# Optimization experiments

Measured on AMD Instinct MI355X. Metric: run time of the kernel, lower is better.

Reference implementation:

```python
import jax, jax.numpy as jnp
import numpy as np
import math

B, Hs, Ws, C, NH, PP = 4, 32, 32, 1024, 16, 128
N = Hs * Ws
HD = C // NH
MAX_REL = 32
ROPE_THETA = 10000.0


def _gelu(t):
    return jax.nn.gelu(t, approximate=False)  # torch nn.GELU default (erf)


def _rope(x):
    # x: [B, nh, N, hd]; interleaved even/odd rotation as in _apply_rope
    hd = x.shape[-1]
    inv_freq = 1.0 / (ROPE_THETA ** (jnp.arange(0, hd, 2, dtype=jnp.float32) / hd))
    pos = jnp.arange(x.shape[-2], dtype=jnp.float32)
    ang = pos[:, None] * inv_freq[None, :]  # [N, hd/2]
    sin, cos = jnp.sin(ang), jnp.cos(ang)
    x1, x2 = x[..., 0::2], x[..., 1::2]
    return jnp.stack([x1 * cos - x2 * sin, x2 * cos + x1 * sin], axis=-1).reshape(x.shape)


def _rel_bias(table):
    # static index computation (numpy), gather from learned table -> [1, NH, N, N]
    coords = np.arange(Hs)
    cy, cx = np.meshgrid(coords, coords, indexing='ij')
    cf = np.stack([cy.reshape(-1), cx.reshape(-1)])  # [2, N]
    rel = cf[:, :, None] - cf[:, None, :]            # [2, N, N]
    idx = (rel[0] + MAX_REL - 1) * (2 * MAX_REL - 1) + (rel[1] + MAX_REL - 1)
    return table[jnp.asarray(idx.reshape(-1))].reshape(N, N, NH).transpose(2, 0, 1)[None]


def setup_inputs() -> dict:
    key = jax.random.key(0)
    ks = iter(jax.random.split(key, 40))
    def w(shape, s=0.02):
        return jax.random.normal(next(ks), shape, jnp.float32) * s
    return dict(
        x=jax.random.normal(next(ks), (B, N, C), jnp.float32),
        plucker=jax.random.normal(next(ks), (B, Hs, Ws, 6), jnp.float32),
        w_qkv=w((C, 3 * C)), w_self_proj=w((C, C)), b_self_proj=jnp.zeros((C,), jnp.float32),
        pl_w1=w((6, 2 * PP)), pl_b1=jnp.zeros((2 * PP,), jnp.float32),
        pl_w2=w((2 * PP, PP)), pl_b2=jnp.zeros((PP,), jnp.float32),
        pl_w3=w((PP, PP)), pl_b3=jnp.zeros((PP,), jnp.float32),
        w_cq=w((C, C)), w_pk=w((PP, C)), w_pv=w((PP, C)),
        w_cross_proj=w((C, C)), b_cross_proj=jnp.zeros((C,), jnp.float32),
        ray_dir_bias=w((NH,)),
        ds_w1=w((6, 4 * NH)), ds_b1=jnp.zeros((4 * NH,), jnp.float32),
        ds_w2=w((4 * NH, NH)), ds_b2=jnp.zeros((NH,), jnp.float32),
        gb_w1=w((2 * PP, C // 2)), gb_b1=jnp.zeros((C // 2,), jnp.float32),
        gb_w2=w((C // 2, NH)), gb_b2=jnp.zeros((NH,), jnp.float32),
        rel_table=w(((2 * MAX_REL - 1) ** 2, NH)),
        gfe_w1=w((C + PP, C)), gfe_b1=jnp.zeros((C,), jnp.float32),
        gfe_w2=w((C, C)), gfe_b2=jnp.zeros((C,), jnp.float32),
    )


def reference(x, plucker, w_qkv, w_self_proj, b_self_proj,
              pl_w1, pl_b1, pl_w2, pl_b2, pl_w3, pl_b3,
              w_cq, w_pk, w_pv, w_cross_proj, b_cross_proj,
              ray_dir_bias, ds_w1, ds_b1, ds_w2, ds_b2,
              gb_w1, gb_b1, gb_w2, gb_b2, rel_table,
              gfe_w1, gfe_b1, gfe_w2, gfe_b2):
    scale = HD ** (-0.5)
    pl_flat = plucker.reshape(B, N, 6)

    # ---- self attention with RoPE + relative position bias ----
    qkv = (x @ w_qkv).reshape(B, N, 3, NH, HD).transpose(2, 0, 3, 1, 4)
    q, k, v = qkv[0], qkv[1], qkv[2]          # [B, NH, N, HD]
    q, k = _rope(q), _rope(k)
    attn = jnp.einsum('bhnd,bhmd->bhnm', q, k) * scale + _rel_bias(rel_table)
    attn = jax.nn.softmax(attn, axis=-1)
    sa = jnp.einsum('bhnm,bhmd->bhnd', attn, v).transpose(0, 2, 1, 3).reshape(B, N, C)
    sa = sa @ w_self_proj + b_self_proj

    # ---- plucker mlp embedding ----
    pp = _gelu(pl_flat @ pl_w1 + pl_b1)
    pp = _gelu(pp @ pl_w2 + pl_b2)
    pp = pp @ pl_w3 + pl_b3                   # [B, N, PP]

    # ---- cross attention (features -> plucker) with geometric biases ----
    cq = (sa @ w_cq).reshape(B, N, NH, HD).transpose(0, 2, 1, 3)
    ck = (pp @ w_pk).reshape(B, N, NH, HD).transpose(0, 2, 1, 3)
    cv = (pp @ w_pv).reshape(B, N, NH, HD).transpose(0, 2, 1, 3)
    cq, ck = _rope(cq), _rope(ck)
    ca = jnp.einsum('bhnd,bhmd->bhnm', cq, ck) * scale

    # ray direction similarity bias (per-head learned weight)
    d = pl_flat[..., :3]
    dn = d / jnp.maximum(jnp.linalg.norm(d, axis=-1, keepdims=True), 1e-12)
    sim = jnp.einsum('bnd,bmd->bnm', dn, dn)  # [B, N, N]
    ca = ca + sim[:, None, :, :] * ray_dir_bias[None, :, None, None]

    # distance-aware per-query multiplicative scale
    ds = jnp.tanh(_gelu(pl_flat @ ds_w1 + ds_b1) @ ds_w2 + ds_b2)  # [B, N, NH]
    ca = ca * (1.0 + ds.transpose(0, 2, 1)[..., None])

    # geometric attention bias from spatial diffs of plucker features
    p2 = pp.reshape(B, Hs, Ws, PP)
    hdiff = jnp.pad(jnp.abs(p2[:, :, 1:] - p2[:, :, :-1]), ((0, 0), (0, 0), (0, 1), (0, 0)))
    vdiff = jnp.pad(jnp.abs(p2[:, 1:] - p2[:, :-1]), ((0, 0), (0, 1), (0, 0), (0, 0)))
    sd = jnp.concatenate([hdiff, vdiff], axis=-1).reshape(B, N, 2 * PP)
    gb = jnp.tanh(_gelu(sd @ gb_w1 + gb_b1) @ gb_w2 + gb_b2)  # [B, N, NH]
    ca = ca + gb.transpose(0, 2, 1)[:, :, None, :]            # broadcast over queries

    ca = jax.nn.softmax(ca, axis=-1)
    co = jnp.einsum('bhnm,bhmd->bhnd', ca, cv).transpose(0, 2, 1, 3).reshape(B, N, C)
    co = co @ w_cross_proj + b_cross_proj

    # ---- geometric feature enhancement + residual ----
    enh = _gelu(jnp.concatenate([co, pp], axis=-1) @ gfe_w1 + gfe_b1) @ gfe_w2 + gfe_b2
    return enh + x
```

## Files before the change

kernel.cpp:

```cpp
#include <hip/hip_runtime.h>
#include <math.h>

#define B_ 4
#define N_ 1024
#define C_ 1024
#define NH_ 16
#define HD_ 64
#define PP_ 128
#define LOG2E 1.4426950408889634f

typedef __bf16 bf16;
typedef __attribute__((ext_vector_type(8))) __bf16 bf16x8;
typedef __attribute__((ext_vector_type(4))) __bf16 bf16x4;
typedef __attribute__((ext_vector_type(4))) float f32x4;

#define MFMA_BF16(a, b, c) __builtin_amdgcn_mfma_f32_16x16x32_bf16((a), (b), (c), 0, 0, 0)

__device__ __forceinline__ float gelu_f(float x) {
    return 0.5f * x * (1.0f + erff(x * 0.70710678118654752f));
}

__device__ __forceinline__ void gload16(const void* g, void* l) {
    __builtin_amdgcn_global_load_lds(
        (const __attribute__((address_space(1))) void*)g,
        (__attribute__((address_space(3))) void*)l, 16, 0, 0);
}

__device__ __forceinline__ void stage64(const bf16* __restrict__ g, int pitchB,
                                        bf16* lds, int t) {
    int row = t >> 3, c = t & 7;
    const char* src = (const char*)g + (size_t)row * pitchB + ((c ^ (row & 7)) << 4);
    gload16(src, lds + (size_t)(t & 448) * 8);
}

__device__ __forceinline__ void stage32(const bf16* __restrict__ g, bf16* lds, int t) {
    if (t < 256) {
        int row = t >> 3, c = t & 7;
        const char* src = (const char*)g + (size_t)row * 128 + ((c ^ (row & 7)) << 4);
        gload16(src, lds + (size_t)(t & 192) * 8);
    }
}

__device__ __forceinline__ bf16x8 lds8_swz(const bf16* lds, int row, int colb) {
    return *reinterpret_cast<const bf16x8*>(
        (const char*)lds + row * 128 + (colb ^ ((row & 7) << 4)));
}

__device__ __forceinline__ bf16x8 lds8_swz256(const bf16* lds, int row, int colb) {
    return *reinterpret_cast<const bf16x8*>(
        (const char*)lds + row * 256 + (colb ^ ((row & 7) << 4)));
}

__device__ __forceinline__ bf16x8 lds8_ke(const bf16* lds, int kr, int g) {
    int r = kr >> 1;
    int ch = ((kr & 1) * 4 + g) ^ (r & 7);
    return *reinterpret_cast<const bf16x8*>((const char*)lds + r * 128 + (ch << 4));
}

__global__ __launch_bounds__(256) void rope_tab_k(float2* __restrict__ rt)
{
    int g = blockIdx.x * 256 + threadIdx.x;
    const int n = g >> 5, i = g & 31;
    const float inv = powf(10000.0f, -(float)(2 * i) / 64.0f);
    const float ang = (float)n * inv;
    rt[g] = make_float2(cosf(ang), sinf(ang));
}

__global__ __launch_bounds__(256) void relT_k(const float* __restrict__ rel_table,
                                              float* __restrict__ relT)
{
    int g = blockIdx.x * 256 + threadIdx.x;
    if (g >= 16 * 3969) return;
    int h = g / 3969, idx = g - h * 3969;
    relT[g] = rel_table[idx * 16 + h];
}

struct TJobs {
    const float* src[11];
    bf16* dst[11];
    int K[11];
    int N[11];
};

__global__ __launch_bounds__(256) void tcast_k(TJobs J)
{
    const int j = blockIdx.z;
    const int Kd = J.K[j], Nd = J.N[j];
    const int n0 = blockIdx.x * 32, k0 = blockIdx.y * 32;
    if (n0 >= Nd || k0 >= Kd) return;
    __shared__ float tl[32][33];
    const int t = threadIdx.x, tx = t & 31, ty = t >> 5;
    const float* src = J.src[j];
    bf16* dst = J.dst[j];
    #pragma unroll
    for (int r = 0; r < 4; ++r) {
        int kk = ty + r * 8;
        tl[kk][tx] = src[(size_t)(k0 + kk) * Nd + n0 + tx];
    }
    __syncthreads();
    #pragma unroll
    for (int r = 0; r < 4; ++r) {
        int nn = ty + r * 8;
        dst[(size_t)(n0 + nn) * Kd + k0 + tx] = (bf16)tl[tx][nn];
    }
}

__global__ __launch_bounds__(256) void cast_rm(const float* __restrict__ in,
                                               bf16* __restrict__ out, int n4)
{
    int g = blockIdx.x * 256 + threadIdx.x;
    if (g >= n4) return;
    float4 v = reinterpret_cast<const float4*>(in)[g];
    bf16x4 o = {(bf16)v.x, (bf16)v.y, (bf16)v.z, (bf16)v.w};
    reinterpret_cast<bf16x4*>(out)[g] = o;
}

template<int NI, int BK>
__global__ __launch_bounds__(256) void gemm_m(
    const bf16* __restrict__ A, const bf16* __restrict__ A2,
    const bf16* __restrict__ Bt, const bf16* __restrict__ Bt2,
    const float* __restrict__ bias, const float* __restrict__ resid,
    void* __restrict__ out0, void* __restrict__ out1, void* __restrict__ out2,
    const float2* __restrict__ rtab,
    int M, int N, int K, int K1A, int K1B, int epi, int act_gelu, float scale)
{
    __shared__ bf16 As[2][128 * BK];
    __shared__ bf16 Bs[2][NI * 32 * BK];
    const int t = threadIdx.x;
    const int w = t >> 6, lane = t & 63;
    const int row0 = blockIdx.y * 128, col0 = blockIdx.x * (NI * 32);
    const int wm = w >> 1, wn = w & 1;
    const int K2A = K - K1A, K2B = K - K1B;
    f32x4 acc[4][NI];
    #pragma unroll
    for (int mi = 0; mi < 4; ++mi)
        #pragma unroll
        for (int ni = 0; ni < NI; ++ni)
            acc[mi][ni] = (f32x4){0.f, 0.f, 0.f, 0.f};

    #define STAGE_AB32(k0, buf)                                                \
        {                                                                      \
            _Pragma("unroll")                                                  \
            for (int r = 0; r < 2; ++r) {                                      \
                int c = r * 256 + t;                                           \
                int rr = c >> 2, koff = (c & 3) * 8;                           \
                const bf16* srca = ((k0) < K1A)                                \
                    ? A + (size_t)(row0 + rr) * K1A + (k0) + koff              \
                    : A2 + (size_t)(row0 + rr) * K2A + ((k0) - K1A) + koff;    \
                gload16(srca, As[buf] + (size_t)(r * 256 + (t & 192)) * 8);    \
            }                                                                  \
            _Pragma("unroll")                                                  \
            for (int r = 0; r < NI / 2; ++r) {                                 \
                int c = r * 256 + t;                                           \
                int rr = c >> 2, koff = (c & 3) * 8;                           \
                const bf16* srcb = ((k0) < K1B)                                \
                    ? Bt + (size_t)(col0 + rr) * K1B + (k0) + koff             \
                    : Bt2 + (size_t)(col0 + rr) * K2B + ((k0) - K1B) + koff;   \
                gload16(srcb, Bs[buf] + (size_t)(r * 256 + (t & 192)) * 8);    \
            }                                                                  \
        }

    #define STAGE_AB64(k0, buf)                                                \
        {                                                                      \
            const bf16* abase; int apitch;                                     \
            if ((k0) < K1A) { abase = A + (k0); apitch = K1A; }                \
            else            { abase = A2 + ((k0) - K1A); apitch = K2A; }       \
            _Pragma("unroll")                                                  \
            for (int r = 0; r < 4; ++r) {                                      \
                int c = r * 256 + t;                                           \
                int rr = c >> 3, cc = c & 7;                                   \
                const char* srca = (const char*)(abase + (size_t)(row0 + rr) * apitch) \
                                   + ((cc ^ (rr & 7)) << 4);                   \
                gload16(srca, As[buf] + (size_t)(r * 256 + (t & 192)) * 8);    \
            }                                                                  \
            const bf16* bbase; int bpitch;                                     \
            if ((k0) < K1B) { bbase = Bt + (k0); bpitch = K1B; }               \
            else            { bbase = Bt2 + ((k0) - K1B); bpitch = K2B; }      \
            _Pragma("unroll")                                                  \
            for (int r = 0; r < NI; ++r) {                                     \
                int c = r * 256 + t;                                           \
                int rr = c >> 3, cc = c & 7;                                   \
                const char* srcb = (const char*)(bbase + (size_t)(col0 + rr) * bpitch) \
                                   + ((cc ^ (rr & 7)) << 4);                   \
                gload16(srcb, Bs[buf] + (size_t)(r * 256 + (t & 192)) * 8);    \
            }                                                                  \
        }

    int cur = 0;
    const int nk = K / BK;
    if constexpr (BK == 32) {
        STAGE_AB32(0, 0);
        __syncthreads();
        for (int kk = 0; kk < nk; ++kk) {
            if (kk + 1 < nk) STAGE_AB32((kk + 1) * 32, cur ^ 1);
            bf16x8 af[4], bfv[NI];
            #pragma unroll
            for (int mi = 0; mi < 4; ++mi)
                af[mi] = *reinterpret_cast<const bf16x8*>(
                    As[cur] + (wm * 64 + mi * 16 + (lane & 15)) * 32 + (lane >> 4) * 8);
            #pragma unroll
            for (int ni = 0; ni < NI; ++ni)
                bfv[ni] = *reinterpret_cast<const bf16x8*>(
                    Bs[cur] + (wn * (NI * 16) + ni * 16 + (lane & 15)) * 32 + (lane >> 4) * 8);
            #pragma unroll
            for (int mi = 0; mi < 4; ++mi)
                #pragma unroll
                for (int ni = 0; ni < NI; ++ni)
                    acc[mi][ni] = MFMA_BF16(af[mi], bfv[ni], acc[mi][ni]);
            __syncthreads();
            cur ^= 1;
        }
    } else {
        STAGE_AB64(0, 0);
        __syncthreads();
        for (int kk = 0; kk < nk; ++kk) {
            if (kk + 1 < nk) STAGE_AB64((kk + 1) * 64, cur ^ 1);
            bf16x8 af[4][2], bfv[NI][2];
            #pragma unroll
            for (int mi = 0; mi < 4; ++mi)
                #pragma unroll
                for (int kh = 0; kh < 2; ++kh)
                    af[mi][kh] = lds8_swz(As[cur], wm * 64 + mi * 16 + (lane & 15),
                                          kh * 64 + (lane >> 4) * 16);
            #pragma unroll
            for (int ni = 0; ni < NI; ++ni)
                #pragma unroll
                for (int kh = 0; kh < 2; ++kh)
                    bfv[ni][kh] = lds8_swz(Bs[cur], wn * (NI * 16) + ni * 16 + (lane & 15),
                                           kh * 64 + (lane >> 4) * 16);
            #pragma unroll
            for (int kh = 0; kh < 2; ++kh)
                #pragma unroll
                for (int mi = 0; mi < 4; ++mi)
                    #pragma unroll
                    for (int ni = 0; ni < NI; ++ni)
                        acc[mi][ni] = MFMA_BF16(af[mi][kh], bfv[ni][kh], acc[mi][ni]);
            __syncthreads();
            cur ^= 1;
        }
    }
    #undef STAGE_AB32
    #undef STAGE_AB64

    #pragma unroll
    for (int mi = 0; mi < 4; ++mi) {
        #pragma unroll
        for (int ni = 0; ni < NI; ++ni) {
            const int col = col0 + wn * (NI * 16) + ni * 16 + (lane & 15);
            if (epi <= 1 || epi == 5) {
                const float bv = bias ? bias[col] : 0.f;
                #pragma unroll
                for (int j = 0; j < 4; ++j) {
                    const int row = row0 + wm * 64 + mi * 16 + (lane >> 4) * 4 + j;
                    float v = acc[mi][ni][j] + bv;
                    if (act_gelu) v = gelu_f(v);
                    if (epi == 0) {
                        if (resid) v += resid[(size_t)row * N + col];
                        ((float*)out0)[(size_t)row * N + col] = v;
                    } else if (epi == 1) {
                        ((bf16*)out0)[(size_t)row * N + col] = (bf16)v;
                    } else {
                        ((float*)out0)[(size_t)row * N + col] = v;
                        ((bf16*)out1)[(size_t)row * N + col] = (bf16)v;
                    }
                }
            } else if (epi == 2) {
                const int reg = col >> 10;
                const int h = (col >> 6) & 15, d = col & 63;
                if (reg <= 1) {
                    bf16* dst = reg == 0 ? (bf16*)out0 : (bf16*)out1;
                    const float sc = reg == 0 ? scale : 1.0f;
                    #pragma unroll
                    for (int j = 0; j < 4; ++j) {
                        const int row = row0 + wm * 64 + mi * 16 + (lane >> 4) * 4 + j;
                        const int b = row >> 10, n = row & 1023;
                        float v = acc[mi][ni][j];
                        float pv = __shfl_xor(v, 1);
                        float2 cs = rtab[(n << 5) + (d >> 1)];
                        float o = (d & 1) == 0 ? v * cs.x - pv * cs.y
                                               : v * cs.x + pv * cs.y;
                        dst[((size_t)((b * 16 + h) * 1024 + n)) * 64 + d] = (bf16)(o * sc);
                    }
                } else {
                    bf16x4 o4;
                    #pragma unroll
                    for (int j = 0; j < 4; ++j) o4[j] = (bf16)acc[mi][ni][j];
                    const int row = row0 + wm * 64 + mi * 16 + (lane >> 4) * 4;
                    const int b = row >> 10, n = row & 1023;
                    *reinterpret_cast<bf16x4*>(
                        (bf16*)out2 + ((size_t)((b * 16 + h) * 64 + d)) * 1024 + n) = o4;
                }
            } else if (epi == 3 || epi == 6) {
                const int h = (col >> 6) & 15, d = col & 63;
                const float bv = bias ? bias[col] : 0.f;
                #pragma unroll
                for (int j = 0; j < 4; ++j) {
                    const int row = row0 + wm * 64 + mi * 16 + (lane >> 4) * 4 + j;
                    const int b = row >> 10, n = row & 1023;
                    float v = acc[mi][ni][j] + bv;
                    float pv = __shfl_xor(v, 1);
                    float2 cs = rtab[(n << 5) + (d >> 1)];
                    float o = (d & 1) == 0 ? v * cs.x - pv * cs.y
                                           : v * cs.x + pv * cs.y;
                    float sc = scale;
                    if (epi == 6) sc *= 1.0f + resid[(size_t)row * 16 + h];
                    ((bf16*)out0)[((size_t)((b * 16 + h) * 1024 + n)) * 64 + d] = (bf16)(o * sc);
                }
            } else if (epi == 7) {
                const int reg = col >> 10;
                const int h = (col >> 6) & 15, d = col & 63;
                if (reg == 0) {
                    #pragma unroll
                    for (int j = 0; j < 4; ++j) {
                        const int row = row0 + wm * 64 + mi * 16 + (lane >> 4) * 4 + j;
                        const int b = row >> 10, n = row & 1023;
                        float v = acc[mi][ni][j];
                        float pv = __shfl_xor(v, 1);
                        float2 cs = rtab[(n << 5) + (d >> 1)];
                        float o = (d & 1) == 0 ? v * cs.x - pv * cs.y
                                               : v * cs.x + pv * cs.y;
                        ((bf16*)out0)[((size_t)((b * 16 + h) * 1024 + n)) * 64 + d] = (bf16)o;
                    }
                } else {
                    bf16x4 o4;
                    #pragma unroll
                    for (int j = 0; j < 4; ++j) o4[j] = (bf16)acc[mi][ni][j];
                    const int row = row0 + wm * 64 + mi * 16 + (lane >> 4) * 4;
                    const int b = row >> 10, n = row & 1023;
                    *reinterpret_cast<bf16x4*>(
                        (bf16*)out2 + ((size_t)((b * 16 + h) * 64 + d)) * 1024 + n) = o4;
                }
            } else {
                const int h = (col >> 6) & 15, d = col & 63;
                bf16x4 o4;
                #pragma unroll
                for (int j = 0; j < 4; ++j) o4[j] = (bf16)acc[mi][ni][j];
                const int row = row0 + wm * 64 + mi * 16 + (lane >> 4) * 4;
                const int b = row >> 10, n = row & 1023;
                *reinterpret_cast<bf16x4*>(
                    (bf16*)out0 + ((size_t)((b * 16 + h) * 64 + d)) * 1024 + n) = o4;
            }
        }
    }
}

__device__ __forceinline__ void attn_bid(int bid, int& bh, int& r0t) {
    const int xcd = bid & 7, s = bid >> 3;
    bh = (s >> 3) * 8 + xcd;
    r0t = s & 7;
}

__global__ __launch_bounds__(512) void attn_self_m(
    const bf16* __restrict__ qb, const bf16* __restrict__ kb, const bf16* __restrict__ vtb,
    const float* __restrict__ relT, bf16* __restrict__ sab)
{
    __shared__ bf16 Ks[2][64 * 64];
    __shared__ bf16 Vs[2][80 * 64];
    __shared__ bf16 Ps[128 * 64];
    __shared__ float relb[2][320];
    const int t = threadIdx.x, w = t >> 6, lane = t & 63;
    int bh, r0t;
    attn_bid(blockIdx.x, bh, r0t);
    const int b = bh >> 4, h = bh & 15, r0 = r0t * 128;
    const float* relTh = relT + h * 3969;
    const int y0 = r0 >> 5;

    {
        const bf16* g = qb + ((size_t)bh * 1024 + r0) * 64;
        #pragma unroll
        for (int r = 0; r < 2; ++r) {
            int i = r * 512 + t;
            int row = i >> 3, c = i & 7;
            const char* src = (const char*)g + (size_t)row * 128 + ((c ^ (row & 7)) << 4);
            gload16(src, Ps + (size_t)(r * 512 + (t & 448)) * 8);
        }
    }
    __syncthreads();
    bf16x8 aq[2];
    {
        const int qr = w * 16 + (lane & 15);
        aq[0] = lds8_swz(Ps, qr, (lane >> 4) * 16);
        aq[1] = lds8_swz(Ps, qr, 64 + (lane >> 4) * 16);
    }
    for (int i = t; i < 2048; i += 512) {
        int buf = i >> 10, idx = i & 1023;
        int row = 64 + (idx >> 6), col = idx & 63;
        Vs[buf][row * 64 + col] = (row == 64) ? (bf16)1.0f : (bf16)0.0f;
    }
    __syncthreads();
    stage64(kb + (size_t)bh * 65536, 128, Ks[0], t);
    stage64(vtb + (size_t)bh * 65536, 2048, Vs[0], t);
    if (t < 320) relb[0][t] = LOG2E * relTh[(y0 + 30 + (t >> 6)) * 63 + min(t & 63, 62)];

    float m_run[4];
    f32x4 of[4], ofe;
    #pragma unroll
    for (int j = 0; j < 4; ++j) m_run[j] = -3e38f;
    #pragma unroll
    for (int dt = 0; dt < 4; ++dt) of[dt] = (f32x4){0.f, 0.f, 0.f, 0.f};
    ofe = (f32x4){0.f, 0.f, 0.f, 0.f};

    const int qrow_lo = (lane >> 4) * 4;
    int dybase[4];
    #pragma unroll
    for (int j = 0; j < 4; ++j) {
        int qg = r0 + w * 16 + qrow_lo + j;
        dybase[j] = (((qg >> 5) - y0) + 1) * 64 + (qg & 31) + 31;
    }
    __syncthreads();

    int cur = 0;
    for (int mt = 0; mt < 16; ++mt) {
        if (mt < 15) {
            stage64(kb + (size_t)bh * 65536 + (size_t)(mt + 1) * 64 * 64, 128, Ks[cur ^ 1], t);
            stage64(vtb + (size_t)bh * 65536 + (size_t)(mt + 1) * 64, 2048, Vs[cur ^ 1], t);
            if (t < 320)
                relb[cur ^ 1][t] = LOG2E * relTh[(y0 - 2 * (mt + 1) + 30 + (t >> 6)) * 63 + min(t & 63, 62)];
        }
        f32x4 sf[4];
        __builtin_amdgcn_s_setprio(1);
        #pragma unroll
        for (int ct = 0; ct < 4; ++ct) {
            const int kr = ct * 16 + (lane & 15);
            f32x4 a = (f32x4){0.f, 0.f, 0.f, 0.f};
            a = MFMA_BF16(aq[0], lds8_swz(Ks[cur], kr, (lane >> 4) * 16), a);
            a = MFMA_BF16(aq[1], lds8_swz(Ks[cur], kr, 64 + (lane >> 4) * 16), a);
            sf[ct] = a;
        }
        __builtin_amdgcn_s_setprio(0);
        float p[4][4], lmax[4];
        #pragma unroll
        for (int j = 0; j < 4; ++j) lmax[j] = -3e38f;
        #pragma unroll
        for (int ct = 0; ct < 4; ++ct) {
            const int xm = (ct & 1) * 16 + (lane & 15);
            const int ro = (ct >> 1) * 64 + xm;
            #pragma unroll
            for (int j = 0; j < 4; ++j) {
                float s = sf[ct][j] + relb[cur][dybase[j] - ro];
                p[ct][j] = s;
                lmax[j] = fmaxf(lmax[j], s);
            }
        }
        bool need = false;
        #pragma unroll
        for (int j = 0; j < 4; ++j) need |= (lmax[j] > m_run[j] + 8.0f);
        if (__any(need)) {
            float mx[4], alpha[4];
            #pragma unroll
            for (int j = 0; j < 4; ++j) mx[j] = lmax[j];
            #pragma unroll
            for (int d = 1; d < 16; d <<= 1)
                #pragma unroll
                for (int j = 0; j < 4; ++j) mx[j] = fmaxf(mx[j], __shfl_xor(mx[j], d));
            #pragma unroll
            for (int j = 0; j < 4; ++j) {
                float mn = fmaxf(m_run[j], mx[j]);
                alpha[j] = exp2f(m_run[j] - mn);
                m_run[j] = mn;
            }
            #pragma unroll
            for (int dt = 0; dt < 4; ++dt)
                #pragma unroll
                for (int j = 0; j < 4; ++j) of[dt][j] *= alpha[j];
            #pragma unroll
            for (int j = 0; j < 4; ++j) ofe[j] *= alpha[j];
        }
        #pragma unroll
        for (int ct = 0; ct < 4; ++ct)
            #pragma unroll
            for (int j = 0; j < 4; ++j)
                p[ct][j] = exp2f(p[ct][j] - m_run[j]);
        #pragma unroll
        for (int ct = 0; ct < 4; ++ct)
            #pragma unroll
            for (int j = 0; j < 4; ++j) {
                const int prow = w * 16 + qrow_lo + j;
                const int ch = (ct * 2 + ((lane & 15) >> 3)) ^ (prow & 7);
                *reinterpret_cast<bf16*>((char*)Ps + prow * 128 + (ch << 4) + (lane & 7) * 2)
                    = (bf16)p[ct][j];
            }
        asm volatile("s_waitcnt lgkmcnt(0)" ::: "memory");
        __builtin_amdgcn_sched_barrier(0);
        bf16x8 ap0 = lds8_swz(Ps, w * 16 + (lane & 15), (lane >> 4) * 16);
        bf16x8 ap1 = lds8_swz(Ps, w * 16 + (lane & 15), 64 + (lane >> 4) * 16);
        __builtin_amdgcn_s_setprio(1);
        #pragma unroll
        for (int dt = 0; dt < 4; ++dt) {
            const int vr = dt * 16 + (lane & 15);
            of[dt] = MFMA_BF16(ap0, lds8_swz(Vs[cur], vr, (lane >> 4) * 16), of[dt]);
            of[dt] = MFMA_BF16(ap1, lds8_swz(Vs[cur], vr, 64 + (lane >> 4) * 16), of[dt]);
        }
        {
            const int vr = 64 + (lane & 15);
            ofe = MFMA_BF16(ap0, lds8_swz(Vs[cur], vr, (lane >> 4) * 16), ofe);
            ofe = MFMA_BF16(ap1, lds8_swz(Vs[cur], vr, 64 + (lane >> 4) * 16), ofe);
        }
        __builtin_amdgcn_s_setprio(0);
        __syncthreads();
        cur ^= 1;
    }
    float inv[4];
    #pragma unroll
    for (int j = 0; j < 4; ++j) inv[j] = 1.f / __shfl(ofe[j], lane & 48);
    #pragma unroll
    for (int dt = 0; dt < 4; ++dt)
        #pragma unroll
        for (int j = 0; j < 4; ++j)
            sab[((size_t)(b * N_ + r0 + w * 16 + qrow_lo + j)) * C_ + h * 64 + dt * 16 + (lane & 15)] =
                (bf16)(of[dt][j] * inv[j]);
}

__global__ __launch_bounds__(512) void attn_cross_m(
    const bf16* __restrict__ cq, const bf16* __restrict__ qe,
    const bf16* __restrict__ ck, const bf16* __restrict__ ke,
    const bf16* __restrict__ cvt, bf16* __restrict__ cob)
{
    __shared__ bf16 Ks[2][64 * 64];
    __shared__ bf16 Ke[2][32 * 64];
    __shared__ bf16 Vs[2][80 * 64];
    __shared__ bf16 Ps[128 * 64];
    const int t = threadIdx.x, w = t >> 6, lane = t & 63;
    int bh, r0t;
    attn_bid(blockIdx.x, bh, r0t);
    const int b = bh >> 4, h = bh & 15, r0 = r0t * 128;

    {
        const bf16* g = cq + ((size_t)bh * 1024 + r0) * 64;
        #pragma unroll
        for (int r = 0; r < 2; ++r) {
            int i = r * 512 + t;
            int row = i >> 3, c = i & 7;
            const char* src = (const char*)g + (size_t)row * 128 + ((c ^ (row & 7)) << 4);
            gload16(src, Ps + (size_t)(r * 512 + (t & 448)) * 8);
        }
    }
    stage64(qe + ((size_t)bh * 1024 + r0) * 32, 128, Ks[0], t);
    __syncthreads();
    bf16x8 aq[2], aqe;
    {
        const int qr = w * 16 + (lane & 15);
        aq[0] = lds8_swz(Ps, qr, (lane >> 4) * 16);
        aq[1] = lds8_swz(Ps, qr, 64 + (lane >> 4) * 16);
        aqe = lds8_ke(Ks[0], qr, lane >> 4);
    }
    for (int i = t; i < 2048; i += 512) {
        int buf = i >> 10, idx = i & 1023;
        int row = 64 + (idx >> 6), col = idx & 63;
        Vs[buf][row * 64 + col] = (row == 64) ? (bf16)1.0f : (bf16)0.0f;
    }
    __syncthreads();
    stage64(ck + (size_t)bh * 65536, 128, Ks[0], t);
    stage32(ke + (size_t)bh * 32768, Ke[0], t);
    stage64(cvt + (size_t)bh * 65536, 2048, Vs[0], t);

    float m_run[4];
    f32x4 of[4], ofe;
    #pragma unroll
    for (int j = 0; j < 4; ++j) m_run[j] = -3e38f;
    #pragma unroll
    for (int dt = 0; dt < 4; ++dt) of[dt] = (f32x4){0.f, 0.f, 0.f, 0.f};
    ofe = (f32x4){0.f, 0.f, 0.f, 0.f};
    const int qrow_lo = (lane >> 4) * 4;
    __syncthreads();

    int cur = 0;
    for (int mt = 0; mt < 16; ++mt) {
        if (mt < 15) {
            stage64(ck + (size_t)bh * 65536 + (size_t)(mt + 1) * 64 * 64, 128, Ks[cur ^ 1], t);
            stage32(ke + (size_t)bh * 32768 + (size_t)(mt + 1) * 64 * 32, Ke[cur ^ 1], t);
            stage64(cvt + (size_t)bh * 65536 + (size_t)(mt + 1) * 64, 2048, Vs[cur ^ 1], t);
        }
        f32x4 sf[4];
        __builtin_amdgcn_s_setprio(1);
        #pragma unroll
        for (int ct = 0; ct < 4; ++ct) {
            const int kr = ct * 16 + (lane & 15);
            f32x4 a = (f32x4){0.f, 0.f, 0.f, 0.f};
            a = MFMA_BF16(aq[0], lds8_swz(Ks[cur], kr, (lane >> 4) * 16), a);
            a = MFMA_BF16(aq[1], lds8_swz(Ks[cur], kr, 64 + (lane >> 4) * 16), a);
            a = MFMA_BF16(aqe, lds8_ke(Ke[cur], kr, lane >> 4), a);
            sf[ct] = a;
        }
        __builtin_amdgcn_s_setprio(0);
        float lmax[4];
        #pragma unroll
        for (int j = 0; j < 4; ++j)
            lmax[j] = fmaxf(fmaxf(sf[0][j], sf[1][j]), fmaxf(sf[2][j], sf[3][j]));
        bool need = false;
        #pragma unroll
        for (int j = 0; j < 4; ++j) need |= (lmax[j] > m_run[j] + 8.0f);
        if (__any(need)) {
            float mx[4], alpha[4];
            #pragma unroll
            for (int j = 0; j < 4; ++j) mx[j] = lmax[j];
            #pragma unroll
            for (int d = 1; d < 16; d <<= 1)
                #pragma unroll
                for (int j = 0; j < 4; ++j) mx[j] = fmaxf(mx[j], __shfl_xor(mx[j], d));
            #pragma unroll
            for (int j = 0; j < 4; ++j) {
                float mn = fmaxf(m_run[j], mx[j]);
                alpha[j] = exp2f(m_run[j] - mn);
                m_run[j] = mn;
            }
            #pragma unroll
            for (int dt = 0; dt < 4; ++dt)
                #pragma unroll
                for (int j = 0; j < 4; ++j) of[dt][j] *= alpha[j];
            #pragma unroll
            for (int j = 0; j < 4; ++j) ofe[j] *= alpha[j];
        }
        #pragma unroll
        for (int ct = 0; ct < 4; ++ct)
            #pragma unroll
            for (int j = 0; j < 4; ++j)
                sf[ct][j] = exp2f(sf[ct][j] - m_run[j]);
        #pragma unroll
        for (int ct = 0; ct < 4; ++ct)
            #pragma unroll
            for (int j = 0; j < 4; ++j) {
                const int prow = w * 16 + qrow_lo + j;
                const int ch = (ct * 2 + ((lane & 15) >> 3)) ^ (prow & 7);
                *reinterpret_cast<bf16*>((char*)Ps + prow * 128 + (ch << 4) + (lane & 7) * 2)
                    = (bf16)sf[ct][j];
            }
        asm volatile("s_waitcnt lgkmcnt(0)" ::: "memory");
        __builtin_amdgcn_sched_barrier(0);
        bf16x8 ap0 = lds8_swz(Ps, w * 16 + (lane & 15), (lane >> 4) * 16);
        bf16x8 ap1 = lds8_swz(Ps, w * 16 + (lane & 15), 64 + (lane >> 4) * 16);
        __builtin_amdgcn_s_setprio(1);
        #pragma unroll
        for (int dt = 0; dt < 4; ++dt) {
            const int vr = dt * 16 + (lane & 15);
            of[dt] = MFMA_BF16(ap0, lds8_swz(Vs[cur], vr, (lane >> 4) * 16), of[dt]);
            of[dt] = MFMA_BF16(ap1, lds8_swz(Vs[cur], vr, 64 + (lane >> 4) * 16), of[dt]);
        }
        {
            const int vr = 64 + (lane & 15);
            ofe = MFMA_BF16(ap0, lds8_swz(Vs[cur], vr, (lane >> 4) * 16), ofe);
            ofe = MFMA_BF16(ap1, lds8_swz(Vs[cur], vr, 64 + (lane >> 4) * 16), ofe);
        }
        __builtin_amdgcn_s_setprio(0);
        __syncthreads();
        cur ^= 1;
    }
    float inv[4];
    #pragma unroll
    for (int j = 0; j < 4; ++j) inv[j] = 1.f / __shfl(ofe[j], lane & 48);
    #pragma unroll
    for (int dt = 0; dt < 4; ++dt)
        #pragma unroll
        for (int j = 0; j < 4; ++j)
            cob[((size_t)(b * N_ + r0 + w * 16 + qrow_lo + j)) * C_ + h * 64 + dt * 16 + (lane & 15)] =
                (bf16)(of[dt][j] * inv[j]);
}

__global__ __launch_bounds__(256) void plucker1_k(
    const float* __restrict__ pl,
    const float* __restrict__ w1, const float* __restrict__ b1,
    const float* __restrict__ dw1, const float* __restrict__ db1,
    const float* __restrict__ dw2, const float* __restrict__ db2,
    bf16* __restrict__ h1b, float* __restrict__ ds, float* __restrict__ dn)
{
    const int t = threadIdx.x;
    __shared__ float plr[6];
    __shared__ float dh[64];
    #pragma unroll 1
    for (int rr = 0; rr < 4; ++rr) {
        const int row = blockIdx.x * 4 + rr;
        if (t < 6) plr[t] = pl[(size_t)row * 6 + t];
        __syncthreads();
        {
            float a = b1[t];
            #pragma unroll
            for (int j = 0; j < 6; ++j) a = fmaf(plr[j], w1[j * 256 + t], a);
            h1b[(size_t)row * 256 + t] = (bf16)gelu_f(a);
        }
        if (t < 64) {
            float d = db1[t];
            #pragma unroll
            for (int j = 0; j < 6; ++j) d = fmaf(plr[j], dw1[j * 64 + t], d);
            dh[t] = gelu_f(d);
        }
        if (t == 0) {
            float x = plr[0], y = plr[1], z = plr[2];
            float nrm = fmaxf(sqrtf(x * x + y * y + z * z), 1e-12f);
            dn[(size_t)row * 4 + 0] = x / nrm;
            dn[(size_t)row * 4 + 1] = y / nrm;
            dn[(size_t)row * 4 + 2] = z / nrm;
            dn[(size_t)row * 4 + 3] = 0.f;
        }
        __syncthreads();
        if (t < 16) {
            float d = db2[t];
            #pragma unroll 8
            for (int j = 0; j < 64; ++j) d = fmaf(dh[j], dw2[j * 16 + t], d);
            ds[(size_t)row * 16 + t] = tanhf(d);
        }
        __syncthreads();
    }
}

__global__ __launch_bounds__(256) void pl23m_k(
    const bf16* __restrict__ h1, const bf16* __restrict__ w2T, const float* __restrict__ b2,
    const bf16* __restrict__ w3T, const float* __restrict__ b3,
    float* __restrict__ pp, bf16* __restrict__ ppb)
{
    __shared__ bf16 Am[64 * 128];
    __shared__ bf16 Wm[128 * 128];
    const int t = threadIdx.x, w = t >> 6, lane = t & 63;
    const int row0 = blockIdx.x * 64;
    f32x4 acc[8];
    #pragma unroll
    for (int nt = 0; nt < 8; ++nt) acc[nt] = (f32x4){0.f, 0.f, 0.f, 0.f};

    for (int kc = 0; kc < 2; ++kc) {
        #pragma unroll
        for (int r = 0; r < 4; ++r) {
            int i = r * 256 + t;
            int row = i >> 4, c = i & 15;
            const char* src = (const char*)(h1 + (size_t)(row0 + row) * 256 + kc * 128)
                              + ((c ^ (row & 7)) << 4);
            gload16(src, Am + (size_t)(r * 256 + (t & 192)) * 8);
        }
        #pragma unroll
        for (int r = 0; r < 8; ++r) {
            int i = r * 256 + t;
            int row = i >> 4, c = i & 15;
            const char* src = (const char*)(w2T + (size_t)row * 256 + kc * 128)
                              + ((c ^ (row & 7)) << 4);
            gload16(src, Wm + (size_t)(r * 256 + (t & 192)) * 8);
        }
        __syncthreads();
        #pragma unroll
        for (int step = 0; step < 4; ++step) {
            bf16x8 af = lds8_swz256(Am, w * 16 + (lane & 15), step * 64 + (lane >> 4) * 16);
            #pragma unroll
            for (int nt = 0; nt < 8; ++nt) {
                bf16x8 bfv = lds8_swz256(Wm, nt * 16 + (lane & 15), step * 64 + (lane >> 4) * 16);
                acc[nt] = MFMA_BF16(af, bfv, acc[nt]);
            }
        }
        __syncthreads();
    }
    #pragma unroll
    for (int r = 0; r < 8; ++r) {
        int i = r * 256 + t;
        int row = i >> 4, c = i & 15;
        const char* src = (const char*)(w3T + (size_t)row * 128) + ((c ^ (row & 7)) << 4);
        gload16(src, Wm + (size_t)(r * 256 + (t & 192)) * 8);
    }
    #pragma unroll
    for (int nt = 0; nt < 8; ++nt) {
        const int col = nt * 16 + (lane & 15);
        const float bv = b2[col];
        #pragma unroll
        for (int j = 0; j < 4; ++j) {
            const int row = w * 16 + (lane >> 4) * 4 + j;
            const int byte = row * 256 + (((col * 2) & ~15) ^ ((row & 7) << 4)) + ((col * 2) & 15);
            *reinterpret_cast<bf16*>((char*)Am + byte) = (bf16)gelu_f(acc[nt][j] + bv);
        }
    }
    __syncthreads();
    f32x4 acc2[8];
    #pragma unroll
    for (int nt = 0; nt < 8; ++nt) acc2[nt] = (f32x4){0.f, 0.f, 0.f, 0.f};
    #pragma unroll
    for (int step = 0; step < 4; ++step) {
        bf16x8 af = lds8_swz256(Am, w * 16 + (lane & 15), step * 64 + (lane >> 4) * 16);
        #pragma unroll
        for (int nt = 0; nt < 8; ++nt) {
            bf16x8 bfv = lds8_swz256(Wm, nt * 16 + (lane & 15), step * 64 + (lane >> 4) * 16);
            acc2[nt] = MFMA_BF16(af, bfv, acc2[nt]);
        }
    }
    #pragma unroll
    for (int nt = 0; nt < 8; ++nt) {
        const int col = nt * 16 + (lane & 15);
        const float bv = b3[col];
        #pragma unroll
        for (int j = 0; j < 4; ++j) {
            const int row = row0 + w * 16 + (lane >> 4) * 4 + j;
            const float v = acc2[nt][j] + bv;
            pp[(size_t)row * 128 + col] = v;
            ppb[(size_t)row * 128 + col] = (bf16)v;
        }
    }
}

__global__ __launch_bounds__(256) void sd_k(const float* __restrict__ pp, bf16* __restrict__ sd)
{
    int g = blockIdx.x * 256 + threadIdx.x;
    if (g >= B_ * N_ * PP_) return;
    const int c = g & 127;
    const int rown = g >> 7;
    const int n = rown & (N_ - 1);
    const int xx = n & 31, yy = (n >> 5) & 31;
    const float cur = pp[g];
    const float hd = (xx < 31) ? fabsf(pp[g + PP_] - cur) : 0.f;
    const float vd = (yy < 31) ? fabsf(pp[g + 32 * PP_] - cur) : 0.f;
    sd[(size_t)rown * 256 + c] = (bf16)hd;
    sd[(size_t)rown * 256 + 128 + c] = (bf16)vd;
}

__global__ __launch_bounds__(256) void gb2x_k(
    const bf16* __restrict__ h, const float* __restrict__ w2, const float* __restrict__ b2,
    const float* __restrict__ dn, const float* __restrict__ ds, const float* __restrict__ rdb,
    bf16* __restrict__ qe, bf16* __restrict__ ke)
{
    __shared__ float w2s[512 * 16];
    const int t = threadIdx.x;
    for (int i = t; i < 8192; i += 256) w2s[i] = w2[i];
    __syncthreads();
    const int row = blockIdx.x * 16 + (t >> 4);
    const int hh = t & 15;
    const bf16* hr = h + (size_t)row * 512;
    float acc = b2[hh];
    #pragma unroll 8
    for (int j = 0; j < 512; ++j)
        acc = fmaf((float)hr[j], w2s[j * 16 + hh], acc);
    const float gbv = tanhf(acc);
    const int b = row >> 10, n = row & 1023;
    const float c1 = rdb[hh] * LOG2E * (1.0f + ds[(size_t)row * 16 + hh]);
    const float dx = dn[(size_t)row * 4], dy = dn[(size_t)row * 4 + 1], dz = dn[(size_t)row * 4 + 2];
    bf16x8 z = {};
    bf16x8 q0 = z, k0 = z;
    q0[0] = (bf16)(dx * c1); q0[1] = (bf16)(dy * c1); q0[2] = (bf16)(dz * c1); q0[3] = (bf16)1.0f;
    k0[0] = (bf16)dx; k0[1] = (bf16)dy; k0[2] = (bf16)dz; k0[3] = (bf16)(gbv * LOG2E);
    const size_t g = (size_t)(b * 16 + hh) * 1024 + n;
    bf16x8* qp = reinterpret_cast<bf16x8*>(qe + g * 32);
    bf16x8* kp = reinterpret_cast<bf16x8*>(ke + g * 32);
    qp[0] = q0; qp[1] = z; qp[2] = z; qp[3] = z;
    kp[0] = k0; kp[1] = z; kp[2] = z; kp[3] = z;
}

extern "C" void kernel_launch(void* const* d_in, const int* in_sizes, int n_in,
                              void* d_out, int out_size, void* d_ws, size_t ws_size,
                              hipStream_t stream)
{
    const float* x     = (const float*)d_in[0];
    const float* pl    = (const float*)d_in[1];
    const float* w_qkv = (const float*)d_in[2];
    const float* w_sp  = (const float*)d_in[3];
    const float* b_sp  = (const float*)d_in[4];
    const float* pl_w1 = (const float*)d_in[5];
    const float* pl_b1 = (const float*)d_in[6];
    const float* pl_w2 = (const float*)d_in[7];
    const float* pl_b2 = (const float*)d_in[8];
    const float* pl_w3 = (const float*)d_in[9];
    const float* pl_b3 = (const float*)d_in[10];
    const float* w_cq  = (const float*)d_in[11];
    const float* w_pk  = (const float*)d_in[12];
    const float* w_pv  = (const float*)d_in[13];
    const float* w_cp  = (const float*)d_in[14];
    const float* b_cp  = (const float*)d_in[15];
    const float* rdb   = (const float*)d_in[16];
    const float* ds_w1 = (const float*)d_in[17];
    const float* ds_b1 = (const float*)d_in[18];
    const float* ds_w2 = (const float*)d_in[19];
    const float* ds_b2 = (const float*)d_in[20];
    const float* gb_w1 = (const float*)d_in[21];
    const float* gb_b1 = (const float*)d_in[22];
    const float* gb_w2 = (const float*)d_in[23];
    const float* gb_b2 = (const float*)d_in[24];
    const float* rel_t = (const float*)d_in[25];
    const float* gfw1  = (const float*)d_in[26];
    const float* gfb1  = (const float*)d_in[27];
    const float* gfw2  = (const float*)d_in[28];
    const float* gfb2  = (const float*)d_in[29];

    char* W = (char*)d_ws;
    float* out = (float*)d_out;
    const size_t MB = 1ull << 20;
    const size_t KB = 1024;

    bf16* qb     = (bf16*)(W + 0);
    bf16* kb     = (bf16*)(W + 8 * MB);
    bf16* vtb    = (bf16*)(W + 16 * MB);
    bf16* cqb    = qb;
    bf16* ckb    = kb;
    bf16* cvtb   = vtb;
    bf16* xb     = (bf16*)(W + 24 * MB);
    bf16* wqkvT  = (bf16*)(W + 32 * MB);
    bf16* wspT   = (bf16*)(W + 38 * MB);
    bf16* wcqT   = (bf16*)(W + 40 * MB);
    bf16* wpkT   = (bf16*)(W + 42 * MB);
    bf16* wpvT   = (bf16*)(W + 42 * MB + 256 * KB);
    bf16* wcpT   = (bf16*)(W + 43 * MB);
    bf16* gfw1T  = (bf16*)(W + 45 * MB);
    bf16* gfw2T  = (bf16*)(W + 48 * MB);
    bf16* gbw1T  = (bf16*)(W + 50 * MB);
    bf16* plw2T  = (bf16*)(W + 50 * MB + 256 * KB);
    bf16* plw3T  = (bf16*)(W + 50 * MB + 320 * KB);
    bf16* sab    = (bf16*)(W + 51 * MB);
    bf16* cob    = sab;
    bf16* sapb   = (bf16*)(W + 59 * MB);
    bf16* copb   = sapb;
    float* pp    = (float*)(W + 67 * MB);
    bf16* ppb    = (bf16*)(W + 69 * MB);
    bf16* sdb16  = (bf16*)(W + 70 * MB);
    bf16* h1b    = (bf16*)(W + 72 * MB);
    bf16* gbh    = (bf16*)(W + 75 * MB);
    float* dsb   = (float*)(W + 79 * MB);
    float* dnb   = (float*)(W + 79 * MB + 256 * KB);
    float2* rtab = (float2*)(W + 80 * MB);
    float* relTb = (float*)(W + 80 * MB + 256 * KB);
    bf16* hidb   = (bf16*)(W + 81 * MB);
    bf16* qeb    = (bf16*)(W + 89 * MB);
    bf16* keb    = (bf16*)(W + 93 * MB);

    const dim3 blk(256);

    TJobs J;
    J.src[0] = w_qkv; J.dst[0] = wqkvT; J.K[0] = 1024; J.N[0] = 3072;
    J.src[1] = w_sp;  J.dst[1] = wspT;  J.K[1] = 1024; J.N[1] = 1024;
    J.src[2] = w_cq;  J.dst[2] = wcqT;  J.K[2] = 1024; J.N[2] = 1024;
    J.src[3] = w_pk;  J.dst[3] = wpkT;  J.K[3] = 128;  J.N[3] = 1024;
    J.src[4] = w_pv;  J.dst[4] = wpvT;  J.K[4] = 128;  J.N[4] = 1024;
    J.src[5] = w_cp;  J.dst[5] = wcpT;  J.K[5] = 1024; J.N[5] = 1024;
    J.src[6] = gfw1;  J.dst[6] = gfw1T; J.K[6] = 1152; J.N[6] = 1024;
    J.src[7] = gfw2;  J.dst[7] = gfw2T; J.K[7] = 1024; J.N[7] = 1024;
    J.src[8] = gb_w1; J.dst[8] = gbw1T; J.K[8] = 256;  J.N[8] = 512;
    J.src[9] = pl_w2; J.dst[9] = plw2T; J.K[9] = 256;  J.N[9] = 128;
    J.src[10]= pl_w3; J.dst[10]= plw3T; J.K[10]= 128;  J.N[10]= 128;
    tcast_k<<<dim3(96, 36, 11), blk, 0, stream>>>(J);
    cast_rm<<<4096, blk, 0, stream>>>(x, xb, 1048576);
    rope_tab_k<<<128, blk, 0, stream>>>(rtab);
    relT_k<<<249, blk, 0, stream>>>(rel_t, relTb);

    gemm_m<2, 64><<<dim3(48, 32), blk, 0, stream>>>(xb, nullptr, wqkvT, nullptr, nullptr, nullptr,
        qb, kb, vtb, rtab, 4096, 3072, 1024, 1024, 1024, 2, 0, 0.125f * LOG2E);
    attn_self_m<<<512, dim3(512), 0, stream>>>(qb, kb, vtb, relTb, sab);
    gemm_m<2, 64><<<dim3(16, 32), blk, 0, stream>>>(sab, nullptr, wspT, nullptr, b_sp, nullptr,
        sapb, nullptr, nullptr, nullptr, 4096, 1024, 1024, 1024, 1024, 1, 0, 1.f);
    plucker1_k<<<1024, blk, 0, stream>>>(pl, pl_w1, pl_b1,
                                         ds_w1, ds_b1, ds_w2, ds_b2, h1b, dsb, dnb);
    pl23m_k<<<64, blk, 0, stream>>>(h1b, plw2T, pl_b2, plw3T, pl_b3, pp, ppb);
    sd_k<<<2048, blk, 0, stream>>>(pp, sdb16);
    gemm_m<2, 64><<<dim3(8, 32), blk, 0, stream>>>(sdb16, nullptr, gbw1T, nullptr, gb_b1, nullptr,
        gbh, nullptr, nullptr, nullptr, 4096, 512, 256, 256, 256, 1, 1, 1.f);
    gb2x_k<<<256, blk, 0, stream>>>(gbh, gb_w2, gb_b2, dnb, dsb, rdb, qeb, keb);
    gemm_m<2, 64><<<dim3(16, 32), blk, 0, stream>>>(sapb, nullptr, wcqT, nullptr, nullptr, dsb,
        cqb, nullptr, nullptr, rtab, 4096, 1024, 1024, 1024, 1024, 6, 0, 0.125f * LOG2E);
    gemm_m<2, 64><<<dim3(32, 32), blk, 0, stream>>>(ppb, nullptr, wpkT, nullptr, nullptr, nullptr,
        ckb, nullptr, cvtb, rtab, 4096, 2048, 128, 128, 128, 7, 0, 1.f);
    attn_cross_m<<<512, dim3(512), 0, stream>>>(cqb, qeb, ckb, keb, cvtb, cob);
    gemm_m<2, 64><<<dim3(16, 32), blk, 0, stream>>>(cob, nullptr, wcpT, nullptr, b_cp, nullptr,
        copb, nullptr, nullptr, nullptr, 4096, 1024, 1024, 1024, 1024, 1, 0, 1.f);
    gemm_m<2, 64><<<dim3(16, 32), blk, 0, stream>>>(copb, ppb, gfw1T, nullptr, gfb1, nullptr,
        hidb, nullptr, nullptr, nullptr, 4096, 1024, 1152, 1024, 1152, 1, 1, 1.f);
    gemm_m<2, 64><<<dim3(16, 32), blk, 0, stream>>>(hidb, nullptr, gfw2T, nullptr, gfb2, x,
        out, nullptr, nullptr, nullptr, 4096, 1024, 1024, 1024, 1024, 0, 0, 1.f);
}
```

Before: 333.2 us.

## Fold self-attention output projection into cross-query weight via precomputed weight product

Because the self-attention projection is linear and feeds only the cross-query projection, the two weight matrices are multiplied once (a 1024x1024x1024 GEMM) and the bias is folded through w_cq in a small reduction kernel. This removes the 4096x1024x1024 self-projection GEMM and its intermediate buffer, replacing it with weight-only work of a quarter the size. The rope and relative-bias table kernels are also merged into one launch. The combined weight is rounded to bf16 once more, which adds a little numerical error.

```diff
diff --git a/kernel.cpp b/kernel.cpp
--- a/kernel.cpp
+++ b/kernel.cpp
@@ -57,29 +57,47 @@
     return *reinterpret_cast<const bf16x8*>((const char*)lds + r * 128 + (ch << 4));
 }
 
-__global__ __launch_bounds__(256) void rope_tab_k(float2* __restrict__ rt)
+__global__ __launch_bounds__(256) void tabs_k(const float* __restrict__ rel_table,
+                                              float* __restrict__ relT,
+                                              float2* __restrict__ rt)
 {
     int g = blockIdx.x * 256 + threadIdx.x;
-    const int n = g >> 5, i = g & 31;
-    const float inv = powf(10000.0f, -(float)(2 * i) / 64.0f);
-    const float ang = (float)n * inv;
-    rt[g] = make_float2(cosf(ang), sinf(ang));
-}
-
-__global__ __launch_bounds__(256) void relT_k(const float* __restrict__ rel_table,
-                                              float* __restrict__ relT)
-{
-    int g = blockIdx.x * 256 + threadIdx.x;
-    if (g >= 16 * 3969) return;
-    int h = g / 3969, idx = g - h * 3969;
-    relT[g] = rel_table[idx * 16 + h];
+    if (g < 32768) {
+        const int n = g >> 5, i = g & 31;
+        const float inv = powf(10000.0f, -(float)(2 * i) / 64.0f);
+        const float ang = (float)n * inv;
+        rt[g] = make_float2(cosf(ang), sinf(ang));
+    } else {
+        int i = g - 32768;
+        if (i < 16 * 3969) {
+            int h = i / 3969, idx = i - h * 3969;
+            relT[i] = rel_table[idx * 16 + h];
+        }
+    }
+}
+
+__global__ __launch_bounds__(256) void bsc_k(const float* __restrict__ b_sp,
+                                             const float* __restrict__ w_cq,
+                                             float* __restrict__ bsc)
+{
+    __shared__ float red[4][64];
+    const int t = threadIdx.x;
+    const int c = blockIdx.x * 64 + (t & 63);
+    const int js = t >> 6;
+    float a = 0.f;
+    #pragma unroll 8
+    for (int j = js * 256; j < js * 256 + 256; ++j)
+        a = fmaf(b_sp[j], w_cq[(size_t)j * 1024 + c], a);
+    red[js][t & 63] = a;
+    __syncthreads();
+    if (t < 64) bsc[blockIdx.x * 64 + t] = red[0][t] + red[1][t] + red[2][t] + red[3][t];
 }
 
 struct TJobs {
-    const float* src[11];
-    bf16* dst[11];
-    int K[11];
-    int N[11];
+    const float* src[10];
+    bf16* dst[10];
+    int K[10];
+    int N[10];
 };
 
 __global__ __launch_bounds__(256) void tcast_k(TJobs J)
@@ -883,7 +901,7 @@
     bf16* cvtb   = vtb;
     bf16* xb     = (bf16*)(W + 24 * MB);
     bf16* wqkvT  = (bf16*)(W + 32 * MB);
-    bf16* wspT   = (bf16*)(W + 38 * MB);
+    bf16* wspB   = (bf16*)(W + 38 * MB);
     bf16* wcqT   = (bf16*)(W + 40 * MB);
     bf16* wpkT   = (bf16*)(W + 42 * MB);
     bf16* wpvT   = (bf16*)(W + 42 * MB + 256 * KB);
@@ -895,8 +913,7 @@
     bf16* plw3T  = (bf16*)(W + 50 * MB + 320 * KB);
     bf16* sab    = (bf16*)(W + 51 * MB);
     bf16* cob    = sab;
-    bf16* sapb   = (bf16*)(W + 59 * MB);
-    bf16* copb   = sapb;
+    bf16* copb   = (bf16*)(W + 59 * MB);
     float* pp    = (float*)(W + 67 * MB);
     bf16* ppb    = (bf16*)(W + 69 * MB);
     bf16* sdb16  = (bf16*)(W + 70 * MB);
@@ -909,31 +926,33 @@
     bf16* hidb   = (bf16*)(W + 81 * MB);
     bf16* qeb    = (bf16*)(W + 89 * MB);
     bf16* keb    = (bf16*)(W + 93 * MB);
+    bf16* wscT   = (bf16*)(W + 97 * MB);
+    float* bscb  = (float*)(W + 99 * MB);
 
     const dim3 blk(256);
 
     TJobs J;
     J.src[0] = w_qkv; J.dst[0] = wqkvT; J.K[0] = 1024; J.N[0] = 3072;
-    J.src[1] = w_sp;  J.dst[1] = wspT;  J.K[1] = 1024; J.N[1] = 1024;
-    J.src[2] = w_cq;  J.dst[2] = wcqT;  J.K[2] = 1024; J.N[2] = 1024;
-    J.src[3] = w_pk;  J.dst[3] = wpkT;  J.K[3] = 128;  J.N[3] = 1024;
-    J.src[4] = w_pv;  J.dst[4] = wpvT;  J.K[4] = 128;  J.N[4] = 1024;
-    J.src[5] = w_cp;  J.dst[5] = wcpT;  J.K[5] = 1024; J.N[5] = 1024;
-    J.src[6] = gfw1;  J.dst[6] = gfw1T; J.K[6] = 1152; J.N[6] = 1024;
-    J.src[7] = gfw2;  J.dst[7] = gfw2T; J.K[7] = 1024; J.N[7] = 1024;
-    J.src[8] = gb_w1; J.dst[8] = gbw1T; J.K[8] = 256;  J.N[8] = 512;
-    J.src[9] = pl_w2; J.dst[9] = plw2T; J.K[9] = 256;  J.N[9] = 128;
-    J.src[10]= pl_w3; J.dst[10]= plw3T; J.K[10]= 128;  J.N[10]= 128;
-    tcast_k<<<dim3(96, 36, 11), blk, 0, stream>>>(J);
+    J.src[1] = w_cq;  J.dst[1] = wcqT;  J.K[1] = 1024; J.N[1] = 1024;
+    J.src[2] = w_pk;  J.dst[2] = wpkT;  J.K[2] = 128;  J.N[2] = 1024;
+    J.src[3] = w_pv;  J.dst[3] = wpvT;  J.K[3] = 128;  J.N[3] = 1024;
+    J.src[4] = w_cp;  J.dst[4] = wcpT;  J.K[4] = 1024; J.N[4] = 1024;
+    J.src[5] = gfw1;  J.dst[5] = gfw1T; J.K[5] = 1152; J.N[5] = 1024;
+    J.src[6] = gfw2;  J.dst[6] = gfw2T; J.K[6] = 1024; J.N[6] = 1024;
+    J.src[7] = gb_w1; J.dst[7] = gbw1T; J.K[7] = 256;  J.N[7] = 512;
+    J.src[8] = pl_w2; J.dst[8] = plw2T; J.K[8] = 256;  J.N[8] = 128;
+    J.src[9] = pl_w3; J.dst[9] = plw3T; J.K[9] = 128;  J.N[9] = 128;
+    tcast_k<<<dim3(96, 36, 10), blk, 0, stream>>>(J);
     cast_rm<<<4096, blk, 0, stream>>>(x, xb, 1048576);
-    rope_tab_k<<<128, blk, 0, stream>>>(rtab);
-    relT_k<<<249, blk, 0, stream>>>(rel_t, relTb);
+    cast_rm<<<1024, blk, 0, stream>>>(w_sp, wspB, 262144);
+    tabs_k<<<377, blk, 0, stream>>>(rel_t, relTb, rtab);
+    bsc_k<<<16, blk, 0, stream>>>(b_sp, w_cq, bscb);
+    gemm_m<2, 64><<<dim3(16, 8), blk, 0, stream>>>(wcqT, nullptr, wspB, nullptr, nullptr, nullptr,
+        wscT, nullptr, nullptr, nullptr, 1024, 1024, 1024, 1024, 1024, 1, 0, 1.f);
 
     gemm_m<2, 64><<<dim3(48, 32), blk, 0, stream>>>(xb, nullptr, wqkvT, nullptr, nullptr, nullptr,
         qb, kb, vtb, rtab, 4096, 3072, 1024, 1024, 1024, 2, 0, 0.125f * LOG2E);
     attn_self_m<<<512, dim3(512), 0, stream>>>(qb, kb, vtb, relTb, sab);
-    gemm_m<2, 64><<<dim3(16, 32), blk, 0, stream>>>(sab, nullptr, wspT, nullptr, b_sp, nullptr,
-        sapb, nullptr, nullptr, nullptr, 4096, 1024, 1024, 1024, 1024, 1, 0, 1.f);
     plucker1_k<<<1024, blk, 0, stream>>>(pl, pl_w1, pl_b1,
                                          ds_w1, ds_b1, ds_w2, ds_b2, h1b, dsb, dnb);
     pl23m_k<<<64, blk, 0, stream>>>(h1b, plw2T, pl_b2, plw3T, pl_b3, pp, ppb);
@@ -941,7 +960,7 @@
     gemm_m<2, 64><<<dim3(8, 32), blk, 0, stream>>>(sdb16, nullptr, gbw1T, nullptr, gb_b1, nullptr,
         gbh, nullptr, nullptr, nullptr, 4096, 512, 256, 256, 256, 1, 1, 1.f);
     gb2x_k<<<256, blk, 0, stream>>>(gbh, gb_w2, gb_b2, dnb, dsb, rdb, qeb, keb);
-    gemm_m<2, 64><<<dim3(16, 32), blk, 0, stream>>>(sapb, nullptr, wcqT, nullptr, nullptr, dsb,
+    gemm_m<2, 64><<<dim3(16, 32), blk, 0, stream>>>(sab, nullptr, wscT, nullptr, bscb, dsb,
         cqb, nullptr, nullptr, rtab, 4096, 1024, 1024, 1024, 1024, 6, 0, 0.125f * LOG2E);
     gemm_m<2, 64><<<dim3(32, 32), blk, 0, stream>>>(ppb, nullptr, wpkT, nullptr, nullptr, nullptr,
         ckb, nullptr, cvtb, rtab, 4096, 2048, 128, 128, 128, 7, 0, 1.f);
```

Result: slower. 342.6 us (+2.8%).
